# Performance work log

Measured on AMD Instinct MI355X. Metric: run time of the kernel, lower is better.

## Reference

```python
import jax, jax.numpy as jnp
import numpy as np

H = 1024          # hidden_size
NH = 16           # num_heads
NKV = 16          # num_kv_heads
HD = 64           # head_dim
INTER = 2048      # intermediate_size
E = 8             # num_experts
TOPK = 2
EPS = 1e-6


def setup_inputs() -> dict:
    key = jax.random.key(0)
    ks = jax.random.split(key, 8)
    B, S = 4, 1024
    total_qkv = (NH + 2 * NKV) * HD
    return {
        "hidden_states": jax.random.normal(ks[0], (B, S, H), dtype=jnp.float32),
        "attention_mask": jnp.zeros((1, 1, S, S), dtype=jnp.float32),
        "input_layernorm": jnp.ones((H,), dtype=jnp.float32),
        "post_attention_layernorm": jnp.ones((H,), dtype=jnp.float32),
        "qkv_w": jax.random.normal(ks[1], (H, total_qkv), dtype=jnp.float32) * 0.02,
        "o_w": jax.random.normal(ks[2], (NH * HD, H), dtype=jnp.float32) * 0.02,
        "router_w": jax.random.normal(ks[3], (H, E), dtype=jnp.float32) * 0.02,
        "gate_up_proj": jax.random.normal(ks[4], (E, H, 2 * INTER), dtype=jnp.float32) * 0.02,
        "down_proj": jax.random.normal(ks[5], (E, INTER, H), dtype=jnp.float32) * 0.02,
    }


def _rmsnorm(x, w):
    var = jnp.mean(x * x, axis=-1, keepdims=True)
    return x * jax.lax.rsqrt(var + EPS) * w


def _attention_block(x, attention_mask, input_layernorm, qkv_w, o_w):
    B, S, _ = x.shape
    h = _rmsnorm(x, input_layernorm)
    qkv = h @ qkv_w  # [B,S,(NH+2*NKV)*HD]
    tq, tkv = NH * HD, NKV * HD
    q = qkv[..., :tq].reshape(B, S, NH, HD).transpose(0, 2, 1, 3)
    k = qkv[..., tq:tq + tkv].reshape(B, S, NKV, HD).transpose(0, 2, 1, 3)
    v = qkv[..., tq + tkv:].reshape(B, S, NKV, HD).transpose(0, 2, 1, 3)
    scores = jnp.einsum('bhqd,bhkd->bhqk', q, k) / np.sqrt(HD).astype(np.float32)
    scores = scores + attention_mask
    attn = jax.nn.softmax(scores, axis=-1)
    out = jnp.einsum('bhqk,bhkd->bhqd', attn, v)
    out = out.transpose(0, 2, 1, 3).reshape(B, S, NH * HD)
    return out @ o_w


def _moe_block(x, post_attention_layernorm, router_w, gate_up_proj, down_proj):
    B, S, _ = x.shape
    xf = x.reshape(-1, H)                      # [T,H]
    T = xf.shape[0]
    hf = _rmsnorm(xf, post_attention_layernorm)
    logits = hf @ router_w                     # [T,E]
    probs = jax.nn.softmax(logits, axis=-1)
    w, idx = jax.lax.top_k(probs, TOPK)        # [T,TOPK]
    w = w / jnp.sum(w, axis=-1, keepdims=True)
    # combine weights scattered into dense [T,E] (0 for unrouted experts)
    cw = jnp.zeros((T, E), dtype=hf.dtype).at[jnp.arange(T)[:, None], idx].add(w)
    out = jnp.zeros_like(hf)
    for e in range(E):  # fixed small expert loop, fully vectorized over tokens
        gu = hf @ gate_up_proj[e]              # [T,2*INTER]
        g, u = gu[:, :INTER], gu[:, INTER:]
        act = jax.nn.silu(g) * u
        out = out + cw[:, e:e + 1] * (act @ down_proj[e])
    return out.reshape(B, S, H)


def reference(hidden_states, attention_mask, input_layernorm, post_attention_layernorm,
              qkv_w, o_w, router_w, gate_up_proj, down_proj):
    x = hidden_states
    x = x + _attention_block(x, attention_mask, input_layernorm, qkv_w, o_w)
    x = x + _moe_block(x, post_attention_layernorm, router_w, gate_up_proj, down_proj)
    return x
```

## Files before the change

### kernel.cpp

```cpp
#include <hip/hip_runtime.h>
#include <cstdint>
#include <cmath>

#define T_TOK 4096
#define H_DIM 1024
#define QKV_N 3072
#define S_LEN 1024
#define INTER_DIM 2048
#define MAXROWS 9216

typedef unsigned short u16;
using f32x4 = __attribute__((ext_vector_type(4))) float;
using h16x8 = __attribute__((ext_vector_type(8))) _Float16;
using h16x4 = __attribute__((ext_vector_type(4))) _Float16;
using i32x4 = __attribute__((ext_vector_type(4))) int;
using u16x4 = __attribute__((ext_vector_type(4))) u16;

__device__ __forceinline__ float bf2f(u16 u){ return __uint_as_float(((uint32_t)u)<<16); }
__device__ __forceinline__ u16 f2bf(float f){
  uint32_t x = __float_as_uint(f);
  uint32_t r = x + 0x7FFFu + ((x>>16)&1u);
  return (u16)(r>>16);
}
__device__ __forceinline__ f32x4 mfma16(h16x8 a, h16x8 b, f32x4 c){
  return __builtin_amdgcn_mfma_f32_16x16x32_f16(a,b,c,0,0,0);
}
__device__ __forceinline__ float rsqrt_acc(float v){
  float r = rsqrtf(v);
  r = r*(1.5f - 0.5f*v*r*r);
  r = r*(1.5f - 0.5f*v*r*r);
  return r;
}
__device__ __forceinline__ float ldin(const void* p, size_t i, int is32){
  return is32 ? ((const float*)p)[i] : bf2f(((const u16*)p)[i]);
}
__device__ __forceinline__ int kslot_sw(int k, int noct){
  return (k&7) | (((k>>3) ^ (noct&3))<<3);
}

__global__ void k_detect(const uint32_t* __restrict__ x, int* __restrict__ dflag){
  uint32_t u = x[threadIdx.x];
  int e = (u>>23)&0xFF;
  int ok = (e>=103 && e<=150);
  unsigned long long m = __ballot(ok);
  if (threadIdx.x==0) *dflag = (__popcll(m) >= 48) ? 1 : 0;
}

__global__ __launch_bounds__(256) void k_transpose_cast(const void* __restrict__ src,
    _Float16* __restrict__ dst, int R, int C, const int* __restrict__ df){
  const int is32 = *df;
  __shared__ _Float16 tile[32][33];
  int tx = threadIdx.x & 31, ty = threadIdx.x >> 5;
  size_t bo = (size_t)blockIdx.z * R * C;
  int c0 = blockIdx.x<<5, r0 = blockIdx.y<<5;
  #pragma unroll
  for (int i=0;i<4;i++){
    int r = ty + i*8;
    tile[r][tx] = (_Float16)ldin(src, bo + (size_t)(r0+r)*C + (c0+tx), is32);
  }
  __syncthreads();
  #pragma unroll
  for (int i=0;i<4;i++){
    int r = ty + i*8;
    dst[bo + (size_t)(c0+r)*R + (r0+tx)] = tile[tx][r];
  }
}

__global__ __launch_bounds__(256) void k_maskchk(const void* __restrict__ m, int* __restrict__ flag,
                                                 const int* __restrict__ df){
  const int is32 = *df;
  int i = (blockIdx.x*256 + threadIdx.x)*4;
  int nz = 0;
  if (is32){
    f32x4 v = *(const f32x4*)&((const float*)m)[i];
    nz = (v[0]!=0.f)||(v[1]!=0.f)||(v[2]!=0.f)||(v[3]!=0.f);
  } else {
    u16x4 v = *(const u16x4*)&((const u16*)m)[i];
    nz = ((v[0]|v[1]|v[2]|v[3]) & 0x7FFF) != 0;
  }
  if (nz) atomicOr(flag, 1);
}

__global__ __launch_bounds__(256) void k_rms1(const void* __restrict__ x, const void* __restrict__ w,
                                              float* __restrict__ h, const int* __restrict__ df){
  const int is32 = *df;
  int t = blockIdx.x, tid = threadIdx.x;
  size_t base = (size_t)t*H_DIM + tid*4;
  float f[4];
  #pragma unroll
  for (int m=0;m<4;m++) f[m] = ldin(x, base+m, is32);
  float ss = f[0]*f[0] + f[1]*f[1] + f[2]*f[2] + f[3]*f[3];
  #pragma unroll
  for (int off=32; off>0; off>>=1) ss += __shfl_down(ss, off, 64);
  __shared__ float red[4];
  if ((tid & 63) == 0) red[tid>>6] = ss;
  __syncthreads();
  float rstd = rsqrt_acc((red[0]+red[1]+red[2]+red[3]) * (1.0f/H_DIM) + 1e-6f);
  f32x4 o;
  #pragma unroll
  for (int m=0;m<4;m++) o[m] = f[m]*rstd*ldin(w, tid*4+m, is32);
  *(f32x4*)&h[base] = o;
}

template<int EPI>
__global__ __launch_bounds__(256) void k_gemm_splitA(const float* __restrict__ A,
    const _Float16* __restrict__ Bt, float* __restrict__ C, const void* __restrict__ res,
    int N, int K, const int* __restrict__ df){
  const int is32 = *df;
  __shared__ __align__(16) _Float16 Ahi[128*32];
  __shared__ __align__(16) _Float16 Alo[128*32];
  __shared__ __align__(16) _Float16 Bs[128*32];
  int tid = threadIdx.x, lane = tid&63, wvx = tid>>6;
  int wr = wvx>>1, wc = wvx&1, quad = lane>>4, lrow = lane&15;
  int m0 = blockIdx.y<<7, n0 = blockIdx.x<<7;
  f32x4 acc[4][4] = {};
  for (int k0=0; k0<K; k0+=32){
    #pragma unroll
    for (int it=0; it<4; it++){
      int ch = it*256 + tid;
      int r = ch>>3, g = ch&7;
      f32x4 v = *(const f32x4*)&A[(size_t)(m0+r)*K + k0 + g*4];
      h16x4 hi, lo;
      #pragma unroll
      for (int q2=0;q2<4;q2++){
        _Float16 hh = (_Float16)v[q2];
        hi[q2] = hh;
        lo[q2] = (_Float16)(v[q2] - (float)hh);
      }
      *(h16x4*)&Ahi[r*32 + g*4] = hi;
      *(h16x4*)&Alo[r*32 + g*4] = lo;
    }
    #pragma unroll
    for (int it=0; it<2; it++){
      int ch = it*256 + tid;
      *(i32x4*)&Bs[ch*8] = *(const i32x4*)&Bt[(size_t)(n0 + (ch>>2))*K + k0 + (ch&3)*8];
    }
    __syncthreads();
    h16x8 ah[4], al[4], bb[4];
    #pragma unroll
    for (int i=0;i<4;i++){
      ah[i] = *(const h16x8*)&Ahi[(wr*64 + i*16 + lrow)*32 + quad*8];
      al[i] = *(const h16x8*)&Alo[(wr*64 + i*16 + lrow)*32 + quad*8];
    }
    #pragma unroll
    for (int j=0;j<4;j++) bb[j] = *(const h16x8*)&Bs[(wc*64 + j*16 + lrow)*32 + quad*8];
    #pragma unroll
    for (int i=0;i<4;i++)
      #pragma unroll
      for (int j=0;j<4;j++){
        acc[i][j] = mfma16(ah[i], bb[j], acc[i][j]);
        acc[i][j] = mfma16(al[i], bb[j], acc[i][j]);
      }
    __syncthreads();
  }
  #pragma unroll
  for (int i=0;i<4;i++)
    #pragma unroll
    for (int j=0;j<4;j++){
      int col = n0 + wc*64 + j*16 + lrow;
      #pragma unroll
      for (int r=0;r<4;r++){
        int row = m0 + wr*64 + i*16 + quad*4 + r;
        size_t idx = (size_t)row*N + col;
        float v = acc[i][j][r];
        if (EPI==1) v += ldin(res, idx, is32);
        C[idx] = v;
      }
    }
}

__global__ __launch_bounds__(256) void k_attn(const float* __restrict__ qkv, const void* __restrict__ mask,
                                              const int* __restrict__ mflag, float* __restrict__ aout,
                                              const int* __restrict__ df){
  const int is32 = *df;
  __shared__ __align__(16) _Float16 Qhi[2*128*32], Qlo[2*128*32];
  __shared__ __align__(16) _Float16 Khi[2*32*32],  Klo[2*32*32];
  __shared__ __align__(16) _Float16 Vhi[64*32],    Vlo[64*32];
  __shared__ __align__(16) _Float16 Phi[128*32],   Plo[128*32];
  int qt = blockIdx.x, bh = blockIdx.y;
  int b = bh>>4, h = bh&15;
  int tid = threadIdx.x, lane = tid&63, wvx = tid>>6, quad = lane>>4, lrow = lane&15;
  size_t tok0 = (size_t)b*S_LEN;
  int q0 = qt<<7;
  #pragma unroll
  for (int it=0; it<8; it++){
    int idx = it*256 + tid;
    int r = idx>>4, g = idx&15;
    int d0 = g*4, p = g>>3;
    f32x4 v = *(const f32x4*)&qkv[(tok0 + q0 + r)*QKV_N + h*64 + d0];
    h16x4 hi, lo;
    #pragma unroll
    for (int m=0;m<4;m++){ _Float16 hh=(_Float16)v[m]; hi[m]=hh; lo[m]=(_Float16)(v[m]-(float)hh); }
    *(h16x4*)&Qhi[(p*128 + r)*32 + (d0&31)] = hi;
    *(h16x4*)&Qlo[(p*128 + r)*32 + (d0&31)] = lo;
  }
  int useMask = *mflag;
  float mrun[2][4], lrun[2][4];
  f32x4 oacc[2][4] = {};
  #pragma unroll
  for (int i=0;i<2;i++)
    #pragma unroll
    for (int r=0;r<4;r++){ mrun[i][r] = -INFINITY; lrun[i][r] = 0.f; }

  for (int kt=0; kt<32; kt++){
    int key0 = kt*32;
    __syncthreads();
    #pragma unroll
    for (int it=0; it<2; it++){
      int idx = it*256 + tid;
      int key = idx>>4, g = idx&15;
      int d0 = g*4, p = g>>3;
      f32x4 v = *(const f32x4*)&qkv[(tok0 + key0 + key)*QKV_N + 1024 + h*64 + d0];
      h16x4 hi, lo;
      #pragma unroll
      for (int m=0;m<4;m++){ _Float16 hh=(_Float16)v[m]; hi[m]=hh; lo[m]=(_Float16)(v[m]-(float)hh); }
      *(h16x4*)&Khi[(p*32 + key)*32 + (d0&31)] = hi;
      *(h16x4*)&Klo[(p*32 + key)*32 + (d0&31)] = lo;
    }
    #pragma unroll
    for (int it=0; it<2; it++){
      int idx = it*256 + tid;
      int key = idx & 31, dg = idx >> 5;
      int d0 = dg*4;
      f32x4 v = *(const f32x4*)&qkv[(tok0 + key0 + key)*QKV_N + 2048 + h*64 + d0];
      #pragma unroll
      for (int m=0;m<4;m++){
        _Float16 hh = (_Float16)v[m];
        Vhi[(d0+m)*32 + key] = hh;
        Vlo[(d0+m)*32 + key] = (_Float16)(v[m]-(float)hh);
      }
    }
    __syncthreads();
    f32x4 sacc[2][2] = {};
    #pragma unroll
    for (int p=0;p<2;p++){
      h16x8 qh[2], ql[2], kh[2], kl[2];
      #pragma unroll
      for (int i=0;i<2;i++){
        qh[i] = *(const h16x8*)&Qhi[(p*128 + wvx*32 + i*16 + lrow)*32 + quad*8];
        ql[i] = *(const h16x8*)&Qlo[(p*128 + wvx*32 + i*16 + lrow)*32 + quad*8];
      }
      #pragma unroll
      for (int j=0;j<2;j++){
        kh[j] = *(const h16x8*)&Khi[(p*32 + j*16 + lrow)*32 + quad*8];
        kl[j] = *(const h16x8*)&Klo[(p*32 + j*16 + lrow)*32 + quad*8];
      }
      #pragma unroll
      for (int i=0;i<2;i++)
        #pragma unroll
        for (int j=0;j<2;j++){
          sacc[i][j] = mfma16(qh[i], kh[j], sacc[i][j]);
          sacc[i][j] = mfma16(qh[i], kl[j], sacc[i][j]);
          sacc[i][j] = mfma16(ql[i], kh[j], sacc[i][j]);
        }
    }
    #pragma unroll
    for (int i=0;i<2;i++){
      #pragma unroll
      for (int r=0;r<4;r++){
        int qrow = q0 + wvx*32 + i*16 + quad*4 + r;
        #pragma unroll
        for (int j=0;j<2;j++){
          float s = sacc[i][j][r] * 0.125f;
          if (useMask) s += ldin(mask, (size_t)qrow*S_LEN + key0 + j*16 + lrow, is32);
          sacc[i][j][r] = s;
        }
        float mx = fmaxf(sacc[i][0][r], sacc[i][1][r]);
        #pragma unroll
        for (int mm=1; mm<=8; mm<<=1) mx = fmaxf(mx, __shfl_xor(mx, mm, 64));
        float mnew = fmaxf(mrun[i][r], mx);
        float alpha = __expf(mrun[i][r] - mnew);
        float ps = 0.f;
        #pragma unroll
        for (int j=0;j<2;j++){
          float p = __expf(sacc[i][j][r] - mnew);
          sacc[i][j][r] = p;
          ps += p;
        }
        #pragma unroll
        for (int mm=1; mm<=8; mm<<=1) ps += __shfl_xor(ps, mm, 64);
        lrun[i][r] = lrun[i][r]*alpha + ps;
        mrun[i][r] = mnew;
        #pragma unroll
        for (int j=0;j<4;j++) oacc[i][j][r] *= alpha;
        int prow = wvx*32 + i*16 + quad*4 + r;
        #pragma unroll
        for (int j=0;j<2;j++){
          int key = j*16 + lrow;
          float pv = sacc[i][j][r];
          _Float16 ph = (_Float16)pv;
          Phi[prow*32 + key] = ph;
          Plo[prow*32 + key] = (_Float16)(pv - (float)ph);
        }
      }
    }
    __syncthreads();
    {
      h16x8 pf[2], pl[2], vh[4], vl[4];
      #pragma unroll
      for (int i=0;i<2;i++){
        pf[i] = *(const h16x8*)&Phi[(wvx*32 + i*16 + lrow)*32 + quad*8];
        pl[i] = *(const h16x8*)&Plo[(wvx*32 + i*16 + lrow)*32 + quad*8];
      }
      #pragma unroll
      for (int j=0;j<4;j++){
        vh[j] = *(const h16x8*)&Vhi[(j*16 + lrow)*32 + quad*8];
        vl[j] = *(const h16x8*)&Vlo[(j*16 + lrow)*32 + quad*8];
      }
      #pragma unroll
      for (int i=0;i<2;i++)
        #pragma unroll
        for (int j=0;j<4;j++){
          oacc[i][j] = mfma16(pf[i], vh[j], oacc[i][j]);
          oacc[i][j] = mfma16(pf[i], vl[j], oacc[i][j]);
          oacc[i][j] = mfma16(pl[i], vh[j], oacc[i][j]);
        }
    }
  }
  #pragma unroll
  for (int i=0;i<2;i++)
    #pragma unroll
    for (int j=0;j<4;j++)
      #pragma unroll
      for (int r=0;r<4;r++){
        int row = q0 + wvx*32 + i*16 + quad*4 + r;
        int col = h*64 + j*16 + lrow;
        aout[(tok0 + row)*H_DIM + col] = oacc[i][j][r] / lrun[i][r];
      }
}

__global__ __launch_bounds__(256) void k_rms2_router(const float* __restrict__ x1, const void* __restrict__ w,
    const void* __restrict__ rw, _Float16* __restrict__ h2,
    int* __restrict__ tok_e, float* __restrict__ tok_w, int* __restrict__ counts,
    const int* __restrict__ df){
  const int is32 = *df;
  int t = blockIdx.x, tid = threadIdx.x;
  f32x4 v = *(const f32x4*)&x1[(size_t)t*H_DIM + tid*4];
  float ss = v[0]*v[0]+v[1]*v[1]+v[2]*v[2]+v[3]*v[3];
  #pragma unroll
  for (int off=32; off>0; off>>=1) ss += __shfl_down(ss, off, 64);
  __shared__ float red[4];
  __shared__ float lgs[32];
  if ((tid&63)==0) red[tid>>6] = ss;
  __syncthreads();
  float rstd = rsqrt_acc((red[0]+red[1]+red[2]+red[3])*(1.0f/H_DIM) + 1e-6f);
  float hv[4];
  h16x4 hst;
  #pragma unroll
  for (int m=0;m<4;m++){ hv[m] = v[m]*rstd*ldin(w, tid*4+m, is32); hst[m] = (_Float16)hv[m]; }
  *(h16x4*)&h2[(size_t)t*H_DIM + tid*4] = hst;
  float part[8] = {0,0,0,0,0,0,0,0};
  #pragma unroll
  for (int m=0;m<4;m++){
    size_t c = (size_t)(tid*4 + m)*8;
    #pragma unroll
    for (int e=0;e<8;e++) part[e] += hv[m]*ldin(rw, c+e, is32);
  }
  #pragma unroll
  for (int e=0;e<8;e++){
    #pragma unroll
    for (int off=32; off>0; off>>=1) part[e] += __shfl_down(part[e], off, 64);
  }
  if ((tid&63)==0){
    #pragma unroll
    for (int e=0;e<8;e++) lgs[(tid>>6)*8 + e] = part[e];
  }
  __syncthreads();
  if (tid==0){
    float lg[8];
    #pragma unroll
    for (int e=0;e<8;e++) lg[e] = lgs[e] + lgs[8+e] + lgs[16+e] + lgs[24+e];
    int e0 = 0;
    #pragma unroll
    for (int e=1;e<8;e++) if (lg[e] > lg[e0]) e0 = e;
    int e1 = (e0==0) ? 1 : 0;
    #pragma unroll
    for (int e=0;e<8;e++) if (e != e0 && lg[e] > lg[e1]) e1 = e;
    float d = expf(lg[e1] - lg[e0]);
    float w0 = 1.0f/(1.0f + d);
    float w1 = d * w0;
    tok_e[t*2] = e0; tok_e[t*2+1] = e1;
    tok_w[t*2] = w0; tok_w[t*2+1] = w1;
    atomicAdd(&counts[e0], 1);
    atomicAdd(&counts[e1], 1);
  }
}

__global__ void k_offsets(const int* __restrict__ counts, int* __restrict__ offs, int* __restrict__ fillpos){
  if (threadIdx.x == 0 && blockIdx.x == 0){
    int o = 0;
    for (int e=0;e<8;e++){
      offs[e] = o; fillpos[e] = o;
      o += (counts[e] + 127) & ~127;
    }
    offs[8] = o;
  }
}

__global__ __launch_bounds__(256) void k_fill(const int* __restrict__ tok_e, const float* __restrict__ tok_w,
    int* __restrict__ fillpos, int* __restrict__ list_ts, float* __restrict__ list_w){
  int t = blockIdx.x*256 + threadIdx.x;
  if (t >= T_TOK) return;
  #pragma unroll
  for (int s=0;s<2;s++){
    int e = tok_e[t*2+s];
    int p = atomicAdd(&fillpos[e], 1);
    list_ts[p] = t*2 + s;
    list_w[p] = tok_w[t*2+s];
  }
}

__global__ __launch_bounds__(256) void k_gemm_gu(const _Float16* __restrict__ h2, const void* __restrict__ guw,
    _Float16* __restrict__ act, const int* __restrict__ list_ts,
    const int* __restrict__ counts, const int* __restrict__ offs, const int* __restrict__ df){
  const int is32 = *df;
  int m0 = blockIdx.y<<7;
  if (m0 >= offs[8]) return;
  int e = 0;
  while (m0 >= offs[e+1]) e++;
  int base = offs[e], cnt = counts[e];
  if (m0 >= base + cnt) return;
  __shared__ __align__(16) _Float16 As[128*32], Bg[64*40], Bu[64*40];
  __shared__ int rowtok[128];
  int tid = threadIdx.x;
  if (tid < 128){
    int mc = min(m0 + tid, base + cnt - 1);
    rowtok[tid] = list_ts[mc] >> 1;
  }
  __syncthreads();
  int lane = tid&63, wvx = tid>>6, wr = wvx>>1, wc = wvx&1, quad = lane>>4, lrow = lane&15;
  int n0 = blockIdx.x<<6;
  size_t ebase = (size_t)e*H_DIM*4096;
  f32x4 ag[4][2] = {}, au[4][2] = {};
  for (int k0=0; k0<1024; k0+=32){
    #pragma unroll
    for (int it=0; it<2; it++){
      int ch = it*256 + tid;
      int r = ch>>2, c = ch&3;
      *(i32x4*)&As[ch*8] = *(const i32x4*)&h2[(size_t)rowtok[r]*H_DIM + k0 + c*8];
    }
    {
      int k = tid>>3, g = tid&7;
      size_t rowb = ebase + (size_t)(k0+k)*4096;
      int ks = kslot_sw(k, g);
      _Float16 tg[8], tu[8];
      if (is32){
        const float* gf = (const float*)guw;
        f32x4 a0 = *(const f32x4*)&gf[rowb + n0 + g*8];
        f32x4 a1 = *(const f32x4*)&gf[rowb + n0 + g*8 + 4];
        f32x4 b0 = *(const f32x4*)&gf[rowb + 2048 + n0 + g*8];
        f32x4 b1 = *(const f32x4*)&gf[rowb + 2048 + n0 + g*8 + 4];
        #pragma unroll
        for (int i=0;i<4;i++){ tg[i]=(_Float16)a0[i]; tg[4+i]=(_Float16)a1[i];
                               tu[i]=(_Float16)b0[i]; tu[4+i]=(_Float16)b1[i]; }
      } else {
        const u16* gb = (const u16*)guw;
        u16x4 a0 = *(const u16x4*)&gb[rowb + n0 + g*8];
        u16x4 a1 = *(const u16x4*)&gb[rowb + n0 + g*8 + 4];
        u16x4 b0 = *(const u16x4*)&gb[rowb + 2048 + n0 + g*8];
        u16x4 b1 = *(const u16x4*)&gb[rowb + 2048 + n0 + g*8 + 4];
        #pragma unroll
        for (int i=0;i<4;i++){ tg[i]=(_Float16)bf2f(a0[i]); tg[4+i]=(_Float16)bf2f(a1[i]);
                               tu[i]=(_Float16)bf2f(b0[i]); tu[4+i]=(_Float16)bf2f(b1[i]); }
      }
      #pragma unroll
      for (int i=0;i<8;i++){
        int n = g*8 + i;
        Bg[n*40 + ks] = tg[i];
        Bu[n*40 + ks] = tu[i];
      }
    }
    __syncthreads();
    h16x8 a[4], bg[2], bu[2];
    #pragma unroll
    for (int i=0;i<4;i++) a[i] = *(const h16x8*)&As[(wr*64 + i*16 + lrow)*32 + quad*8];
    #pragma unroll
    for (int j=0;j<2;j++){
      int n = wc*32 + j*16 + lrow;
      int oct = (quad ^ ((n>>3)&3))*8;
      bg[j] = *(const h16x8*)&Bg[n*40 + oct];
      bu[j] = *(const h16x8*)&Bu[n*40 + oct];
    }
    #pragma unroll
    for (int i=0;i<4;i++)
      #pragma unroll
      for (int j=0;j<2;j++){
        ag[i][j] = mfma16(a[i], bg[j], ag[i][j]);
        au[i][j] = mfma16(a[i], bu[j], au[i][j]);
      }
    __syncthreads();
  }
  #pragma unroll
  for (int i=0;i<4;i++)
    #pragma unroll
    for (int j=0;j<2;j++)
      #pragma unroll
      for (int r=0;r<4;r++){
        int row = m0 + wr*64 + i*16 + quad*4 + r;
        int col = n0 + wc*32 + j*16 + lrow;
        float g = ag[i][j][r], u = au[i][j][r];
        float sv = g / (1.0f + __expf(-g));
        act[(size_t)row*INTER_DIM + col] = (_Float16)(sv * u);
      }
}

__global__ __launch_bounds__(256) void k_gemm_down(const _Float16* __restrict__ act, const void* __restrict__ dw,
    _Float16* __restrict__ slotbuf, const int* __restrict__ list_ts, const float* __restrict__ list_w,
    const int* __restrict__ counts, const int* __restrict__ offs, const int* __restrict__ df){
  const int is32 = *df;
  int m0 = blockIdx.y<<7;
  if (m0 >= offs[8]) return;
  int e = 0;
  while (m0 >= offs[e+1]) e++;
  int base = offs[e], cnt = counts[e];
  if (m0 >= base + cnt) return;
  __shared__ __align__(16) _Float16 As[128*32], Bs[128*40];
  int tid = threadIdx.x, lane = tid&63, wvx = tid>>6;
  int wr = wvx>>1, wc = wvx&1, quad = lane>>4, lrow = lane&15;
  int n0 = blockIdx.x<<7;
  size_t ebase = (size_t)e*INTER_DIM*H_DIM;
  f32x4 acc[4][4] = {};
  for (int k0=0; k0<2048; k0+=32){
    #pragma unroll
    for (int it=0; it<2; it++){
      int ch = it*256 + tid;
      int r = ch>>2, c = ch&3;
      *(i32x4*)&As[ch*8] = *(const i32x4*)&act[(size_t)(m0+r)*INTER_DIM + k0 + c*8];
    }
    {
      int k = tid>>3, g = tid&7;
      size_t rowb = ebase + (size_t)(k0+k)*H_DIM;
      int ks = kslot_sw(k, g);
      #pragma unroll
      for (int p=0;p<2;p++){
        _Float16 tb[8];
        if (is32){
          const float* bf = (const float*)dw;
          f32x4 a0 = *(const f32x4*)&bf[rowb + n0 + p*64 + g*8];
          f32x4 a1 = *(const f32x4*)&bf[rowb + n0 + p*64 + g*8 + 4];
          #pragma unroll
          for (int i=0;i<4;i++){ tb[i]=(_Float16)a0[i]; tb[4+i]=(_Float16)a1[i]; }
        } else {
          const u16* bb = (const u16*)dw;
          u16x4 a0 = *(const u16x4*)&bb[rowb + n0 + p*64 + g*8];
          u16x4 a1 = *(const u16x4*)&bb[rowb + n0 + p*64 + g*8 + 4];
          #pragma unroll
          for (int i=0;i<4;i++){ tb[i]=(_Float16)bf2f(a0[i]); tb[4+i]=(_Float16)bf2f(a1[i]); }
        }
        #pragma unroll
        for (int i=0;i<8;i++){
          int n = p*64 + g*8 + i;
          Bs[n*40 + ks] = tb[i];
        }
      }
    }
    __syncthreads();
    h16x8 a[4], b[4];
    #pragma unroll
    for (int i=0;i<4;i++) a[i] = *(const h16x8*)&As[(wr*64 + i*16 + lrow)*32 + quad*8];
    #pragma unroll
    for (int j=0;j<4;j++){
      int n = wc*64 + j*16 + lrow;
      b[j] = *(const h16x8*)&Bs[n*40 + ((quad ^ ((n>>3)&3))*8)];
    }
    #pragma unroll
    for (int i=0;i<4;i++)
      #pragma unroll
      for (int j=0;j<4;j++)
        acc[i][j] = mfma16(a[i], b[j], acc[i][j]);
    __syncthreads();
  }
  #pragma unroll
  for (int i=0;i<4;i++)
    #pragma unroll
    for (int r=0;r<4;r++){
      int m = m0 + wr*64 + i*16 + quad*4 + r;
      if (m < base + cnt){
        int ts = list_ts[m];
        float wgt = list_w[m];
        #pragma unroll
        for (int j=0;j<4;j++){
          int col = n0 + wc*64 + j*16 + lrow;
          slotbuf[(size_t)ts*H_DIM + col] = (_Float16)(wgt * acc[i][j][r]);
        }
      }
    }
}

__global__ __launch_bounds__(256) void k_final(const float* __restrict__ x1, const _Float16* __restrict__ slot,
                                               void* __restrict__ outv, const int* __restrict__ df){
  const int is32 = *df;
  int i4 = (blockIdx.x*256 + threadIdx.x)*4;
  int t = i4 >> 10, c = i4 & 1023;
  f32x4 a = *(const f32x4*)&x1[i4];
  h16x4 s0 = *(const h16x4*)&slot[(size_t)(t*2)*H_DIM + c];
  h16x4 s1 = *(const h16x4*)&slot[(size_t)(t*2+1)*H_DIM + c];
  if (is32){
    f32x4 o;
    #pragma unroll
    for (int m=0;m<4;m++) o[m] = a[m] + (float)s0[m] + (float)s1[m];
    *(f32x4*)&((float*)outv)[i4] = o;
  } else {
    u16x4 o;
    #pragma unroll
    for (int m=0;m<4;m++) o[m] = f2bf(a[m] + (float)s0[m] + (float)s1[m]);
    *(u16x4*)&((u16*)outv)[i4] = o;
  }
}

extern "C" void kernel_launch(void* const* d_in, const int* in_sizes, int n_in,
                              void* d_out, int out_size, void* d_ws, size_t ws_size,
                              hipStream_t stream){
  (void)in_sizes; (void)n_in; (void)out_size; (void)ws_size;
  const void* x    = d_in[0];
  const void* mask = d_in[1];
  const void* ln1  = d_in[2];
  const void* ln2  = d_in[3];
  const void* qkvw = d_in[4];
  const void* ow   = d_in[5];
  const void* rw   = d_in[6];
  const void* guw  = d_in[7];
  const void* dww  = d_in[8];

  char* ws = (char*)d_ws;
  size_t off = 0;
  auto alloc = [&](size_t b)->void*{ void* p = ws + off; off = (off + b + 255) & ~(size_t)255; return p; };
  int* meta            = (int*)alloc(32*sizeof(int));
  _Float16* qkv_wt     = (_Float16*)alloc((size_t)3072*1024*2);
  _Float16* o_wt       = (_Float16*)alloc((size_t)1024*1024*2);
  float* hbuf          = (float*)alloc((size_t)4096*1024*4);
  float* qkvbuf        = (float*)alloc((size_t)4096*3072*4);
  float* x1            = (float*)alloc((size_t)4096*1024*4);
  _Float16* slotbuf    = (_Float16*)alloc((size_t)4096*2*1024*2);
  int* list_ts         = (int*)alloc(MAXROWS*4);
  float* list_w        = (float*)alloc(MAXROWS*4);
  int* tok_e           = (int*)alloc((size_t)4096*2*4);
  float* tok_w         = (float*)alloc((size_t)4096*2*4);

  int* counts = meta;
  int* offs   = meta + 8;
  int* fillpos= meta + 17;
  int* flag   = meta + 25;
  int* dflag  = meta + 26;
  _Float16* h2  = (_Float16*)qkvbuf;
  _Float16* act = (_Float16*)((char*)qkvbuf + (size_t)4096*1024*2);

  hipMemsetAsync(meta, 0, 32*sizeof(int), stream);
  k_detect<<<dim3(1), dim3(64), 0, stream>>>((const uint32_t*)x, dflag);
  k_transpose_cast<<<dim3(3072/32, 1024/32, 1), 256, 0, stream>>>(qkvw, qkv_wt, 1024, 3072, dflag);
  k_transpose_cast<<<dim3(1024/32, 1024/32, 1), 256, 0, stream>>>(ow, o_wt, 1024, 1024, dflag);
  k_maskchk<<<dim3(1024), 256, 0, stream>>>(mask, flag, dflag);
  k_rms1<<<dim3(4096), 256, 0, stream>>>(x, ln1, hbuf, dflag);
  k_gemm_splitA<0><<<dim3(24, 32), 256, 0, stream>>>(hbuf, qkv_wt, qkvbuf, nullptr, 3072, 1024, dflag);
  k_attn<<<dim3(8, 64), 256, 0, stream>>>(qkvbuf, mask, flag, hbuf, dflag);
  k_gemm_splitA<1><<<dim3(8, 32), 256, 0, stream>>>(hbuf, o_wt, x1, x, 1024, 1024, dflag);
  k_rms2_router<<<dim3(4096), 256, 0, stream>>>(x1, ln2, rw, h2, tok_e, tok_w, counts, dflag);
  k_offsets<<<dim3(1), dim3(64), 0, stream>>>(counts, offs, fillpos);
  k_fill<<<dim3(16), 256, 0, stream>>>(tok_e, tok_w, fillpos, list_ts, list_w);
  k_gemm_gu<<<dim3(32, 72), 256, 0, stream>>>(h2, guw, act, list_ts, counts, offs, dflag);
  k_gemm_down<<<dim3(8, 72), 256, 0, stream>>>(act, dww, slotbuf, list_ts, list_w, counts, offs, dflag);
  k_final<<<dim3(4096), 256, 0, stream>>>(x1, slotbuf, d_out, dflag);
}
```

Baseline: 965.6 us.

## Pre-transpose MoE expert weights to fp16 and use direct-to-LDS loads

Adds a widened 64x64 transpose-cast kernel and, when the workspace is large enough, converts the gate_up and down expert weights into transposed fp16 copies on every call. New grouped GEMM kernels then read these K-contiguous weights with global_load_lds, and the QKV/O GEMM B-tile loads switch to the same path. This targets the strided, per-element format-converting weight reads in the old expert GEMMs. The cost is an extra full pass over the expert weights each call plus a larger workspace, and slotbuf now aliases hbuf.

```diff
diff --git a/kernel.cpp b/kernel.cpp
--- a/kernel.cpp
+++ b/kernel.cpp
@@ -15,6 +15,7 @@
 using h16x4 = __attribute__((ext_vector_type(4))) _Float16;
 using i32x4 = __attribute__((ext_vector_type(4))) int;
 using u16x4 = __attribute__((ext_vector_type(4))) u16;
+using u16x8 = __attribute__((ext_vector_type(8))) u16;
 
 __device__ __forceinline__ float bf2f(u16 u){ return __uint_as_float(((uint32_t)u)<<16); }
 __device__ __forceinline__ u16 f2bf(float f){
@@ -36,6 +37,11 @@
 }
 __device__ __forceinline__ int kslot_sw(int k, int noct){
   return (k&7) | (((k>>3) ^ (noct&3))<<3);
+}
+__device__ __forceinline__ void gll16(const void* g, void* l){
+  __builtin_amdgcn_global_load_lds(
+      (const __attribute__((address_space(1))) void*)g,
+      (__attribute__((address_space(3))) void*)l, 16, 0, 0);
 }
 
 __global__ void k_detect(const uint32_t* __restrict__ x, int* __restrict__ dflag){
@@ -46,23 +52,39 @@
   if (threadIdx.x==0) *dflag = (__popcll(m) >= 48) ? 1 : 0;
 }
 
-__global__ __launch_bounds__(256) void k_transpose_cast(const void* __restrict__ src,
+__global__ __launch_bounds__(256) void k_trans2(const void* __restrict__ src,
     _Float16* __restrict__ dst, int R, int C, const int* __restrict__ df){
   const int is32 = *df;
-  __shared__ _Float16 tile[32][33];
-  int tx = threadIdx.x & 31, ty = threadIdx.x >> 5;
+  __shared__ _Float16 t[64][65];
   size_t bo = (size_t)blockIdx.z * R * C;
-  int c0 = blockIdx.x<<5, r0 = blockIdx.y<<5;
-  #pragma unroll
-  for (int i=0;i<4;i++){
-    int r = ty + i*8;
-    tile[r][tx] = (_Float16)ldin(src, bo + (size_t)(r0+r)*C + (c0+tx), is32);
+  int c0 = blockIdx.x<<6, r0 = blockIdx.y<<6;
+  int ty = threadIdx.x>>3, tx = threadIdx.x&7;
+  #pragma unroll
+  for (int rr=0; rr<2; rr++){
+    int r = rr*32 + ty;
+    size_t gi = bo + (size_t)(r0+r)*C + c0 + tx*8;
+    _Float16 v[8];
+    if (is32){
+      f32x4 a0 = *(const f32x4*)&((const float*)src)[gi];
+      f32x4 a1 = *(const f32x4*)&((const float*)src)[gi+4];
+      #pragma unroll
+      for (int i=0;i<4;i++){ v[i]=(_Float16)a0[i]; v[4+i]=(_Float16)a1[i]; }
+    } else {
+      u16x8 a = *(const u16x8*)&((const u16*)src)[gi];
+      #pragma unroll
+      for (int i=0;i<8;i++) v[i]=(_Float16)bf2f(a[i]);
+    }
+    #pragma unroll
+    for (int i=0;i<8;i++) t[r][tx*8+i] = v[i];
   }
   __syncthreads();
   #pragma unroll
-  for (int i=0;i<4;i++){
-    int r = ty + i*8;
-    dst[bo + (size_t)(c0+r)*R + (r0+tx)] = tile[tx][r];
+  for (int rr=0; rr<2; rr++){
+    int n = rr*32 + ty;
+    h16x8 v;
+    #pragma unroll
+    for (int i=0;i<8;i++) v[i] = t[tx*8+i][n];
+    *(h16x8*)&dst[bo + (size_t)(c0+n)*R + r0 + tx*8] = v;
   }
 }
 
@@ -133,7 +155,7 @@
     #pragma unroll
     for (int it=0; it<2; it++){
       int ch = it*256 + tid;
-      *(i32x4*)&Bs[ch*8] = *(const i32x4*)&Bt[(size_t)(n0 + (ch>>2))*K + k0 + (ch&3)*8];
+      gll16(&Bt[(size_t)(n0 + (ch>>2))*K + k0 + (ch&3)*8], &Bs[(size_t)(it*256 + wvx*64)*8]);
     }
     __syncthreads();
     h16x8 ah[4], al[4], bb[4];
@@ -409,6 +431,120 @@
     list_w[p] = tok_w[t*2+s];
   }
 }
+
+
+__global__ __launch_bounds__(256) void k_gemm_gu_t(const _Float16* __restrict__ h2,
+    const _Float16* __restrict__ gwt, _Float16* __restrict__ act, const int* __restrict__ list_ts,
+    const int* __restrict__ counts, const int* __restrict__ offs){
+  int m0 = blockIdx.y<<7;
+  if (m0 >= offs[8]) return;
+  int e = 0;
+  while (m0 >= offs[e+1]) e++;
+  int base = offs[e], cnt = counts[e];
+  if (m0 >= base + cnt) return;
+  __shared__ __align__(16) _Float16 As[128*32], Bg[64*32], Bu[64*32];
+  __shared__ int rowtok[128];
+  int tid = threadIdx.x;
+  if (tid < 128) rowtok[tid] = list_ts[min(m0 + tid, base + cnt - 1)] >> 1;
+  __syncthreads();
+  int lane = tid&63, wvx = tid>>6, wr = wvx>>1, wc = wvx&1, quad = lane>>4, lrow = lane&15;
+  int n0 = blockIdx.x<<6;
+  const _Float16* Bge = gwt + (size_t)e*4096*1024 + (size_t)n0*1024;
+  const _Float16* Bue = gwt + (size_t)e*4096*1024 + (size_t)(2048+n0)*1024;
+  const _Float16* arow0 = &h2[(size_t)rowtok[tid>>2]*H_DIM + (tid&3)*8];
+  const _Float16* arow1 = &h2[(size_t)rowtok[(256+tid)>>2]*H_DIM + (tid&3)*8];
+  int bR = tid>>2, bG = tid&3;
+  f32x4 ag[4][2] = {}, au[4][2] = {};
+  for (int k0=0; k0<1024; k0+=32){
+    gll16(arow0 + k0, &As[(size_t)(wvx*64)*8]);
+    gll16(arow1 + k0, &As[(size_t)(256 + wvx*64)*8]);
+    gll16(&Bge[(size_t)bR*1024 + k0 + bG*8], &Bg[(size_t)(wvx*64)*8]);
+    gll16(&Bue[(size_t)bR*1024 + k0 + bG*8], &Bu[(size_t)(wvx*64)*8]);
+    __syncthreads();
+    h16x8 a[4], bg[2], bu[2];
+    #pragma unroll
+    for (int i=0;i<4;i++) a[i] = *(const h16x8*)&As[(wr*64 + i*16 + lrow)*32 + quad*8];
+    #pragma unroll
+    for (int j=0;j<2;j++){
+      bg[j] = *(const h16x8*)&Bg[(wc*32 + j*16 + lrow)*32 + quad*8];
+      bu[j] = *(const h16x8*)&Bu[(wc*32 + j*16 + lrow)*32 + quad*8];
+    }
+    #pragma unroll
+    for (int i=0;i<4;i++)
+      #pragma unroll
+      for (int j=0;j<2;j++){
+        ag[i][j] = mfma16(a[i], bg[j], ag[i][j]);
+        au[i][j] = mfma16(a[i], bu[j], au[i][j]);
+      }
+    __syncthreads();
+  }
+  #pragma unroll
+  for (int i=0;i<4;i++)
+    #pragma unroll
+    for (int j=0;j<2;j++)
+      #pragma unroll
+      for (int r=0;r<4;r++){
+        int row = m0 + wr*64 + i*16 + quad*4 + r;
+        int col = n0 + wc*32 + j*16 + lrow;
+        float g = ag[i][j][r], u = au[i][j][r];
+        float sv = g / (1.0f + __expf(-g));
+        act[(size_t)row*INTER_DIM + col] = (_Float16)(sv * u);
+      }
+}
+
+__global__ __launch_bounds__(256) void k_gemm_down_t(const _Float16* __restrict__ act,
+    const _Float16* __restrict__ dwt, _Float16* __restrict__ slotbuf, const int* __restrict__ list_ts,
+    const float* __restrict__ list_w, const int* __restrict__ counts, const int* __restrict__ offs){
+  int m0 = blockIdx.y<<7;
+  if (m0 >= offs[8]) return;
+  int e = 0;
+  while (m0 >= offs[e+1]) e++;
+  int base = offs[e], cnt = counts[e];
+  if (m0 >= base + cnt) return;
+  __shared__ __align__(16) _Float16 As[128*32], Bs[128*32];
+  int tid = threadIdx.x, lane = tid&63, wvx = tid>>6;
+  int wr = wvx>>1, wc = wvx&1, quad = lane>>4, lrow = lane&15;
+  int n0 = blockIdx.x<<7;
+  const _Float16* Be = dwt + (size_t)e*1024*2048 + (size_t)n0*2048;
+  f32x4 acc[4][4] = {};
+  for (int k0=0; k0<2048; k0+=32){
+    #pragma unroll
+    for (int it=0; it<2; it++){
+      int c2 = it*256 + tid;
+      int r = c2>>2, g = c2&3;
+      gll16(&act[(size_t)(m0+r)*INTER_DIM + k0 + g*8], &As[(size_t)(it*256 + wvx*64)*8]);
+      gll16(&Be[(size_t)r*2048 + k0 + g*8], &Bs[(size_t)(it*256 + wvx*64)*8]);
+    }
+    __syncthreads();
+    h16x8 a[4], b[4];
+    #pragma unroll
+    for (int i=0;i<4;i++) a[i] = *(const h16x8*)&As[(wr*64 + i*16 + lrow)*32 + quad*8];
+    #pragma unroll
+    for (int j=0;j<4;j++) b[j] = *(const h16x8*)&Bs[(wc*64 + j*16 + lrow)*32 + quad*8];
+    #pragma unroll
+    for (int i=0;i<4;i++)
+      #pragma unroll
+      for (int j=0;j<4;j++)
+        acc[i][j] = mfma16(a[i], b[j], acc[i][j]);
+    __syncthreads();
+  }
+  #pragma unroll
+  for (int i=0;i<4;i++)
+    #pragma unroll
+    for (int r=0;r<4;r++){
+      int m = m0 + wr*64 + i*16 + quad*4 + r;
+      if (m < base + cnt){
+        int ts = list_ts[m];
+        float wgt = list_w[m];
+        #pragma unroll
+        for (int j=0;j<4;j++){
+          int col = n0 + wc*64 + j*16 + lrow;
+          slotbuf[(size_t)ts*H_DIM + col] = (_Float16)(wgt * acc[i][j][r]);
+        }
+      }
+    }
+}
+
 
 __global__ __launch_bounds__(256) void k_gemm_gu(const _Float16* __restrict__ h2, const void* __restrict__ guw,
     _Float16* __restrict__ act, const int* __restrict__ list_ts,
@@ -611,7 +747,7 @@
 extern "C" void kernel_launch(void* const* d_in, const int* in_sizes, int n_in,
                               void* d_out, int out_size, void* d_ws, size_t ws_size,
                               hipStream_t stream){
-  (void)in_sizes; (void)n_in; (void)out_size; (void)ws_size;
+  (void)in_sizes; (void)n_in; (void)out_size;
   const void* x    = d_in[0];
   const void* mask = d_in[1];
   const void* ln1  = d_in[2];
@@ -631,24 +767,33 @@
   float* hbuf          = (float*)alloc((size_t)4096*1024*4);
   float* qkvbuf        = (float*)alloc((size_t)4096*3072*4);
   float* x1            = (float*)alloc((size_t)4096*1024*4);
-  _Float16* slotbuf    = (_Float16*)alloc((size_t)4096*2*1024*2);
   int* list_ts         = (int*)alloc(MAXROWS*4);
   float* list_w        = (float*)alloc(MAXROWS*4);
   int* tok_e           = (int*)alloc((size_t)4096*2*4);
   float* tok_w         = (float*)alloc((size_t)4096*2*4);
+  size_t base_end = off;
+  _Float16* gu_wt      = (_Float16*)alloc((size_t)8*4096*1024*2);
+  _Float16* down_wt    = (_Float16*)alloc((size_t)8*1024*2048*2);
+  const int big = (ws_size >= off) ? 1 : 0;
+  (void)base_end;
 
   int* counts = meta;
   int* offs   = meta + 8;
   int* fillpos= meta + 17;
   int* flag   = meta + 25;
   int* dflag  = meta + 26;
-  _Float16* h2  = (_Float16*)qkvbuf;
-  _Float16* act = (_Float16*)((char*)qkvbuf + (size_t)4096*1024*2);
+  _Float16* h2      = (_Float16*)qkvbuf;
+  _Float16* act     = (_Float16*)((char*)qkvbuf + (size_t)4096*1024*2);
+  _Float16* slotbuf = (_Float16*)hbuf;
 
   hipMemsetAsync(meta, 0, 32*sizeof(int), stream);
   k_detect<<<dim3(1), dim3(64), 0, stream>>>((const uint32_t*)x, dflag);
-  k_transpose_cast<<<dim3(3072/32, 1024/32, 1), 256, 0, stream>>>(qkvw, qkv_wt, 1024, 3072, dflag);
-  k_transpose_cast<<<dim3(1024/32, 1024/32, 1), 256, 0, stream>>>(ow, o_wt, 1024, 1024, dflag);
+  k_trans2<<<dim3(48, 16, 1), 256, 0, stream>>>(qkvw, qkv_wt, 1024, 3072, dflag);
+  k_trans2<<<dim3(16, 16, 1), 256, 0, stream>>>(ow, o_wt, 1024, 1024, dflag);
+  if (big){
+    k_trans2<<<dim3(64, 16, 8), 256, 0, stream>>>(guw, gu_wt, 1024, 4096, dflag);
+    k_trans2<<<dim3(16, 32, 8), 256, 0, stream>>>(dww, down_wt, 2048, 1024, dflag);
+  }
   k_maskchk<<<dim3(1024), 256, 0, stream>>>(mask, flag, dflag);
   k_rms1<<<dim3(4096), 256, 0, stream>>>(x, ln1, hbuf, dflag);
   k_gemm_splitA<0><<<dim3(24, 32), 256, 0, stream>>>(hbuf, qkv_wt, qkvbuf, nullptr, 3072, 1024, dflag);
@@ -657,7 +802,12 @@
   k_rms2_router<<<dim3(4096), 256, 0, stream>>>(x1, ln2, rw, h2, tok_e, tok_w, counts, dflag);
   k_offsets<<<dim3(1), dim3(64), 0, stream>>>(counts, offs, fillpos);
   k_fill<<<dim3(16), 256, 0, stream>>>(tok_e, tok_w, fillpos, list_ts, list_w);
-  k_gemm_gu<<<dim3(32, 72), 256, 0, stream>>>(h2, guw, act, list_ts, counts, offs, dflag);
-  k_gemm_down<<<dim3(8, 72), 256, 0, stream>>>(act, dww, slotbuf, list_ts, list_w, counts, offs, dflag);
+  if (big){
+    k_gemm_gu_t<<<dim3(32, 72), 256, 0, stream>>>(h2, gu_wt, act, list_ts, counts, offs);
+    k_gemm_down_t<<<dim3(8, 72), 256, 0, stream>>>(act, down_wt, slotbuf, list_ts, list_w, counts, offs);
+  } else {
+    k_gemm_gu<<<dim3(32, 72), 256, 0, stream>>>(h2, guw, act, list_ts, counts, offs, dflag);
+    k_gemm_down<<<dim3(8, 72), 256, 0, stream>>>(act, dww, slotbuf, list_ts, list_w, counts, offs, dflag);
+  }
   k_final<<<dim3(4096), 256, 0, stream>>>(x1, slotbuf, d_out, dflag);
 }
```

Result: faster. 922.0 us (-4.5%).
